# Performance work log

Measured on AMD Instinct MI355X. Metric: run time of the kernel, lower is better.

## Reference

```python
import jax, jax.numpy as jnp
import numpy as np

EPS = 1e-5
SCALE = 30.0

def _ln(x, g, b):
    mu = jnp.mean(x, -1, keepdims=True)
    var = jnp.mean((x - mu) ** 2, -1, keepdims=True)
    return (x - mu) / jnp.sqrt(var + EPS) * g + b

def _gather_nodes(h_V, E_idx):
    # h_V: [B,N,H], E_idx: [B,N,K] -> [B,N,K,H]
    return jax.vmap(lambda v, i: v[i])(h_V, E_idx)

def setup_inputs() -> dict:
    B, N, K, H, IN = 4, 2048, 48, 128, 128
    key = jax.random.key(0)
    ks = jax.random.split(key, 24)
    def lin(k, din, dout):
        kw, kb = jax.random.split(k)
        return (jax.random.normal(kw, (din, dout), jnp.float32) * 0.02,
                jax.random.normal(kb, (dout,), jnp.float32) * 0.02)
    W1_w, W1_b = lin(ks[0], H + IN, H)
    W2_w, W2_b = lin(ks[1], H, H)
    W3_w, W3_b = lin(ks[2], H, H)
    W11_w, W11_b = lin(ks[3], 2 * H + IN, H)
    W12_w, W12_b = lin(ks[4], H, H)
    W13_w, W13_b = lin(ks[5], H, IN)
    Win_w, Win_b = lin(ks[6], H, 4 * H)
    Wout_w, Wout_b = lin(ks[7], 4 * H, H)
    return {
        'h_V': jax.random.normal(ks[8], (B, N, H), jnp.float32),
        'h_E': jax.random.normal(ks[9], (B, N, K, IN), jnp.float32),
        'mask_V': jnp.ones((B, N), jnp.float32),
        'E_idx': jax.random.randint(ks[10], (B, N, K), 0, N),
        'mask_attend': jax.random.uniform(ks[11], (B, N, K), jnp.float32),
        'W1_w': W1_w, 'W1_b': W1_b, 'W2_w': W2_w, 'W2_b': W2_b,
        'W3_w': W3_w, 'W3_b': W3_b,
        'W11_w': W11_w, 'W11_b': W11_b, 'W12_w': W12_w, 'W12_b': W12_b,
        'W13_w': W13_w, 'W13_b': W13_b,
        'Win_w': Win_w, 'Win_b': Win_b, 'Wout_w': Wout_w, 'Wout_b': Wout_b,
        'ln1_g': jnp.ones((H,), jnp.float32), 'ln1_b': jnp.zeros((H,), jnp.float32),
        'ln2_g': jnp.ones((H,), jnp.float32), 'ln2_b': jnp.zeros((H,), jnp.float32),
        'ln3_g': jnp.ones((IN,), jnp.float32), 'ln3_b': jnp.zeros((IN,), jnp.float32),
    }

def reference(h_V, h_E, mask_V, E_idx, mask_attend,
              W1_w, W1_b, W2_w, W2_b, W3_w, W3_b,
              W11_w, W11_b, W12_w, W12_b, W13_w, W13_b,
              Win_w, Win_b, Wout_w, Wout_b,
              ln1_g, ln1_b, ln2_g, ln2_b, ln3_g, ln3_b):
    K = h_E.shape[-2]
    gelu = jax.nn.gelu
    # node message MLP over concat([h_V expanded, h_E])
    h_V_exp = jnp.broadcast_to(h_V[:, :, None, :], h_E.shape[:3] + (h_V.shape[-1],))
    h_EV = jnp.concatenate([h_V_exp, h_E], -1)  # [B,N,K,H+IN]
    h_msg = gelu(h_EV @ W1_w + W1_b)
    h_msg = gelu(h_msg @ W2_w + W2_b)
    h_msg = h_msg @ W3_w + W3_b
    h_msg = mask_attend[..., None] * h_msg
    dh = jnp.sum(h_msg, -2) / SCALE
    h_V = _ln(h_V + dh, ln1_g, ln1_b)  # dropout is identity in eval
    # FFN
    dh = gelu(h_V @ Win_w + Win_b) @ Wout_w + Wout_b
    h_V = _ln(h_V + dh, ln2_g, ln2_b)
    h_V = mask_V[..., None] * h_V
    # edge update: cat_neighbors_nodes = cat([h_E, gather(h_V, E_idx)], -1)
    h_nbr = _gather_nodes(h_V, E_idx)  # [B,N,K,H]
    h_EV2 = jnp.concatenate([h_E, h_nbr], -1)  # [B,N,K,IN+H]
    h_V_exp2 = jnp.broadcast_to(h_V[:, :, None, :], (h_V.shape[0], h_V.shape[1], K, h_V.shape[-1]))
    h_EV2 = jnp.concatenate([h_V_exp2, h_EV2], -1)  # [B,N,K,2H+IN]
    h_msg2 = gelu(h_EV2 @ W11_w + W11_b)
    h_msg2 = gelu(h_msg2 @ W12_w + W12_b)
    h_msg2 = h_msg2 @ W13_w + W13_b
    h_E = _ln(h_E + h_msg2, ln3_g, ln3_b)
    return (h_V, h_E)
```

## Files before the change

kernel.cpp:

```cpp
#include <hip/hip_runtime.h>
#include <stdint.h>


typedef __attribute__((ext_vector_type(8))) short bf16x8;
typedef __attribute__((ext_vector_type(4))) float f32x4;
typedef __attribute__((ext_vector_type(4))) float vf4;
typedef __attribute__((ext_vector_type(2))) float vf2;

#define MFMA16(a,b,c) __builtin_amdgcn_mfma_f32_16x16x32_bf16((a),(b),(c),0,0,0)
#define PITCH 17

__device__ __forceinline__ float bf2f(uint16_t u){
  union { uint32_t i; float f; } v; v.i = ((uint32_t)u) << 16; return v.f;
}
__device__ __forceinline__ uint32_t cvtpk(float lo, float hi){
  uint32_t r; asm("v_cvt_pk_bf16_f32 %0, %1, %2" : "=v"(r) : "v"(lo), "v"(hi));
  return r;
}
__device__ __forceinline__ uint16_t f2bf1(float x){ return (uint16_t)cvtpk(x, x); }
__device__ __forceinline__ uint4 pk8v(vf4 a, vf4 b){
  uint4 v; v.x=cvtpk(a[0],a[1]); v.y=cvtpk(a[2],a[3]);
  v.z=cvtpk(b[0],b[1]); v.w=cvtpk(b[2],b[3]); return v;
}
__device__ __forceinline__ float geluf(float x){
  float u = 0.7978845608028654f * x * fmaf(0.044715f, x*x, 1.0f);
  float e = __builtin_amdgcn_exp2f(2.8853900817779268f * u);
  float r = __builtin_amdgcn_rcpf(1.0f + e);
  return fmaf(-x, r, x);
}
template<int CTRL>
__device__ __forceinline__ float dpp_add(float x){
  int s = __builtin_amdgcn_update_dpp(0, __builtin_bit_cast(int, x), CTRL, 0xF, 0xF, true);
  return x + __builtin_bit_cast(float, s);
}
__device__ __forceinline__ float red16(float x){
  x = dpp_add<0x121>(x); x = dpp_add<0x122>(x);
  x = dpp_add<0x124>(x); x = dpp_add<0x128>(x);
  return x;
}
__device__ __forceinline__ bf16x8 wfragf(const float* __restrict__ W, int ncols,
                                         int k0, int col, int g){
  const float* p = W + (size_t)(k0 + g*8)*ncols + col;
  bf16x8 f;
#pragma unroll
  for (int j=0;j<8;j++) f[j] = (short)f2bf1(p[j*ncols]);
  return f;
}
__device__ __forceinline__ bf16x8 afrag(const uint4* tile, int row, int s, int g){
  return *(const bf16x8*)&tile[row*PITCH + 4*s + g];
}
__device__ __forceinline__ void st_m(uint4* tile, int row, int col, uint16_t val){
  ((uint16_t*)tile)[row*(PITCH*8) + col] = val;
}

__global__ __launch_bounds__(512) void k_node(
  const float* __restrict__ hV, const float* __restrict__ hE,
  const float* __restrict__ mAtt,
  const float* __restrict__ W1, const float* __restrict__ B1,
  const float* __restrict__ W2, const float* __restrict__ B2,
  const float* __restrict__ W3, const float* __restrict__ B3,
  const float* __restrict__ LG1, const float* __restrict__ LB1,
  float* __restrict__ x1f, uint16_t* __restrict__ x1b)
{
  __shared__ uint4 Ab[2][48*PITCH];
  __shared__ uint4 Cb[48*PITCH];
  __shared__ uint4 hvb[16];
  __shared__ float maskb[48];
  __shared__ float dhb[128];

  const int tid = threadIdx.x;
  const int w = tid >> 6, lane = tid & 63, g = lane >> 4, l15 = lane & 15;
  const int col = w*16 + l15;
  const int row0 = tid>>4, cir = tid&15, row1 = 32 + (tid>>4);

  bf16x8 W1f[8], W2f[4], W3f[4];
#pragma unroll
  for (int s=0;s<8;s++) W1f[s] = wfragf(W1,128,32*s,col,g);
#pragma unroll
  for (int s=0;s<4;s++) W2f[s] = wfragf(W2,128,32*s,col,g);
#pragma unroll
  for (int s=0;s<4;s++) W3f[s] = wfragf(W3,128,32*s,col,g);
  const float b1c = B1[col], b2c = B2[col], b3c = B3[col];

  vf4 sr0, sr1, sr2, sr3, hva, hvc; float mk = 0.f;
  {
    const float* hb = hE + (size_t)(blockIdx.x*8)*6144;
    sr0 = __builtin_nontemporal_load((const vf4*)(hb + tid*8));
    sr1 = __builtin_nontemporal_load((const vf4*)(hb + tid*8 + 4));
    if (tid < 256){
      sr2 = __builtin_nontemporal_load((const vf4*)(hb + 4096 + tid*8));
      sr3 = __builtin_nontemporal_load((const vf4*)(hb + 4096 + tid*8 + 4));
    }
    if (tid < 16){
      const float* p = hV + (size_t)(blockIdx.x*8)*128 + tid*8;
      hva = *(const vf4*)p; hvc = *(const vf4*)(p+4);
    }
    if (tid >= 64 && tid < 112) mk = mAtt[(size_t)(blockIdx.x*8)*48 + (tid-64)];
    Ab[0][row0*PITCH + cir] = pk8v(sr0, sr1);
    if (tid < 256) Ab[0][row1*PITCH + cir] = pk8v(sr2, sr3);
    if (tid < 16) hvb[tid] = pk8v(hva, hvc);
    if (tid >= 64 && tid < 112) maskb[tid-64] = mk;
  }
  __syncthreads();

  for (int it=0; it<8; ++it){
    const int node = blockIdx.x*8 + it;
    const uint4* Ac = Ab[it&1];
    uint4* Acm = Ab[it&1];
    uint4* An  = Ab[(it&1)^1];
    f32x4 ahv = {0,0,0,0};
#pragma unroll
    for (int s=0;s<4;s++) ahv = MFMA16(*(const bf16x8*)&hvb[4*s+g], W1f[s], ahv);
#pragma unroll
    for (int t=0;t<3;t++){
      f32x4 acc = ahv;
      int row = 16*t + l15;
#pragma unroll
      for (int s=0;s<4;s++) acc = MFMA16(afrag(Ac,row,s,g), W1f[4+s], acc);
#pragma unroll
      for (int r=0;r<4;r++) st_m(Cb, 16*t+4*g+r, col, f2bf1(geluf(acc[r]+b1c)));
    }
    __syncthreads();
#pragma unroll
    for (int t=0;t<3;t++){
      f32x4 acc = {0,0,0,0};
      int row = 16*t + l15;
#pragma unroll
      for (int s=0;s<4;s++) acc = MFMA16(afrag(Cb,row,s,g), W2f[s], acc);
#pragma unroll
      for (int r=0;r<4;r++) st_m(Acm, 16*t+4*g+r, col, f2bf1(geluf(acc[r]+b2c)));
    }
    __syncthreads();
    if (it < 7){
      const float* hb = hE + (size_t)(node+1)*6144;
      sr0 = __builtin_nontemporal_load((const vf4*)(hb + tid*8));
      sr1 = __builtin_nontemporal_load((const vf4*)(hb + tid*8 + 4));
      if (tid < 256){
        sr2 = __builtin_nontemporal_load((const vf4*)(hb + 4096 + tid*8));
        sr3 = __builtin_nontemporal_load((const vf4*)(hb + 4096 + tid*8 + 4));
      }
      if (tid < 16){
        const float* p = hV + (size_t)(node+1)*128 + tid*8;
        hva = *(const vf4*)p; hvc = *(const vf4*)(p+4);
      }
      if (tid >= 64 && tid < 112) mk = mAtt[(size_t)(node+1)*48 + (tid-64)];
    }
    float pp = 0.f;
#pragma unroll
    for (int t=0;t<3;t++){
      f32x4 acc = {0,0,0,0};
      int row = 16*t + l15;
#pragma unroll
      for (int s=0;s<4;s++) acc = MFMA16(afrag(Ac,row,s,g), W3f[s], acc);
#pragma unroll
      for (int r=0;r<4;r++) pp += maskb[16*t+4*g+r] * (acc[r] + b3c);
    }
    pp += __shfl_xor(pp, 16);
    pp += __shfl_xor(pp, 32);
    if (lane < 16) dhb[col] = pp * (1.f/30.f);
    __syncthreads();
    if (tid < 64){
      int c0 = 2*tid, c1 = c0+1;
      float2 hv2 = *(const float2*)(hV + (size_t)node*128 + c0);
      float xa = hv2.x + dhb[c0];
      float xc = hv2.y + dhb[c1];
      float s1 = xa + xc, s2 = xa*xa + xc*xc;
      s1 = red16(s1); s2 = red16(s2);
      s1 += __shfl_xor(s1,16); s2 += __shfl_xor(s2,16);
      s1 += __shfl_xor(s1,32); s2 += __shfl_xor(s2,32);
      float mu = s1 * (1.0f/128.0f);
      float var = fmaxf(s2 * (1.0f/128.0f) - mu*mu, 0.f);
      float rstd = __builtin_amdgcn_rsqf(var + 1e-5f);
      float ya = (xa-mu)*rstd*LG1[c0] + LB1[c0];
      float yc = (xc-mu)*rstd*LG1[c1] + LB1[c1];
      float2 o2; o2.x = ya; o2.y = yc;
      ((float2*)x1f)[(size_t)node*64 + tid] = o2;
      ((uint32_t*)x1b)[(size_t)node*64 + tid] = cvtpk(ya, yc);
    }
    if (it < 7){
      An[row0*PITCH + cir] = pk8v(sr0, sr1);
      if (tid < 256) An[row1*PITCH + cir] = pk8v(sr2, sr3);
      if (tid < 16) hvb[tid] = pk8v(hva, hvc);
      if (tid >= 64 && tid < 112) maskb[tid-64] = mk;
    }
    __syncthreads();
  }
}

__global__ __launch_bounds__(512) void k_ffn(
  const float* __restrict__ x1f, const uint16_t* __restrict__ x1b,
  const float* __restrict__ Win, const float* __restrict__ Bin,
  const float* __restrict__ Wout, const float* __restrict__ Bout,
  const float* __restrict__ LG2, const float* __restrict__ LB2,
  const float* __restrict__ maskV,
  float* __restrict__ outV, uint16_t* __restrict__ outVb)
{
  __shared__ uint4 lh[16*65];
  __shared__ float xb[16*129];

  const int tid = threadIdx.x;
  const int w = tid>>6, lane = tid&63, g = lane>>4, l15 = lane&15;
  const int colo = w*16 + l15;

  bf16x8 WiF[4][4], WoF[16];
#pragma unroll
  for (int s=0;s<4;s++)
#pragma unroll
    for (int c=0;c<4;c++) WiF[s][c] = wfragf(Win,512,32*s, w*64 + c*16 + l15, g);
#pragma unroll
  for (int s=0;s<16;s++) WoF[s] = wfragf(Wout,128,32*s, colo, g);
  float binc[4];
#pragma unroll
  for (int c=0;c<4;c++) binc[c] = Bin[w*64 + c*16 + l15];
  const float boutc = Bout[colo];

  for (int it=0; it<2; ++it){
    const int node0 = (blockIdx.x*2 + it)*16;
    bf16x8 A[4];
#pragma unroll
    for (int s=0;s<4;s++) A[s] = *(const bf16x8*)(x1b + (size_t)(node0 + l15)*128 + 32*s + 8*g);
#pragma unroll
    for (int c=0;c<4;c++){
      f32x4 acc = {0,0,0,0};
#pragma unroll
      for (int s=0;s<4;s++) acc = MFMA16(A[s], WiF[s][c], acc);
      int colh = w*64 + c*16 + l15;
#pragma unroll
      for (int r=0;r<4;r++){
        int row = 4*g + r;
        ((uint16_t*)lh)[row*(65*8) + colh] = f2bf1(geluf(acc[r] + binc[c]));
      }
    }
    __syncthreads();
    f32x4 acc = {0,0,0,0};
#pragma unroll
    for (int s=0;s<16;s++){
      bf16x8 a = *(const bf16x8*)&lh[l15*65 + 4*s + g];
      acc = MFMA16(a, WoF[s], acc);
    }
#pragma unroll
    for (int r=0;r<4;r++){
      int row = 4*g + r;
      xb[row*129 + colo] = x1f[(size_t)(node0+row)*128 + colo] + acc[r] + boutc;
    }
    __syncthreads();
#pragma unroll
    for (int rr=0; rr<2; ++rr){
      int row = w + rr*8;
      int c0 = 2*lane, c1 = c0+1;
      float xa = xb[row*129 + c0], xc = xb[row*129 + c1];
      float s1 = xa + xc, s2 = xa*xa + xc*xc;
      s1 = red16(s1); s2 = red16(s2);
      s1 += __shfl_xor(s1,16); s2 += __shfl_xor(s2,16);
      s1 += __shfl_xor(s1,32); s2 += __shfl_xor(s2,32);
      float mu = s1*(1.0f/128.0f);
      float var = fmaxf(s2*(1.0f/128.0f)-mu*mu, 0.f);
      float rstd = __builtin_amdgcn_rsqf(var + 1e-5f);
      float mv = maskV[node0 + row];
      float ya = ((xa-mu)*rstd*LG2[c0] + LB2[c0]) * mv;
      float yc = ((xc-mu)*rstd*LG2[c1] + LB2[c1]) * mv;
      vf2 o2; o2[0] = ya; o2[1] = yc;
      __builtin_nontemporal_store(o2, (vf2*)outV + (size_t)(node0+row)*64 + lane);
      if (outVb)
        ((uint32_t*)outVb)[(size_t)(node0+row)*64 + lane] = cvtpk(ya, yc);
    }
    __syncthreads();
  }
}

template<bool BF16G>
__global__ __launch_bounds__(512) void k_edge(
  const float* __restrict__ hE, const int* __restrict__ Eidx,
  const float* __restrict__ hV2f, const uint16_t* __restrict__ hV2b,
  const float* __restrict__ W11, const float* __restrict__ B11,
  const float* __restrict__ W12, const float* __restrict__ B12,
  const float* __restrict__ W13, const float* __restrict__ B13,
  const float* __restrict__ LG3, const float* __restrict__ LB3,
  float* __restrict__ outE)
{
  __shared__ uint4 Ab[2][48*PITCH];
  __shared__ uint4 Bb[48*PITCH];
  __shared__ uint4 Cb[48*PITCH];
  __shared__ uint4 hvb[16];

  const int tid = threadIdx.x;
  const int w = tid>>6, lane = tid&63, g = lane>>4, l15 = lane&15;
  const int col = w*16 + l15;
  const int row0 = tid>>4, cir = tid&15, row1 = 32 + (tid>>4);

  bf16x8 Ws[4], W11e[4], W11n[4], W12f[4], W13f[4];
#pragma unroll
  for (int s=0;s<4;s++) Ws[s]   = wfragf(W11,128,     32*s,col,g);
#pragma unroll
  for (int s=0;s<4;s++) W11e[s] = wfragf(W11,128, 128+32*s,col,g);
#pragma unroll
  for (int s=0;s<4;s++) W11n[s] = wfragf(W11,128, 256+32*s,col,g);
#pragma unroll
  for (int s=0;s<4;s++) W12f[s] = wfragf(W12,128,     32*s,col,g);
#pragma unroll
  for (int s=0;s<4;s++) W13f[s] = wfragf(W13,128,     32*s,col,g);
  const float b11c = B11[col], b12c = B12[col], b13c = B13[col];

  vf4 sr0, sr1, sr2, sr3; int gi0, gi1; uint4 hvr;
  {
    const int node = blockIdx.x*8;
    const int bb = (node >> 11) << 11;
    const float* hb = hE + (size_t)node*6144;
    sr0 = __builtin_nontemporal_load((const vf4*)(hb + tid*8));
    sr1 = __builtin_nontemporal_load((const vf4*)(hb + tid*8 + 4));
    if (tid < 256){
      sr2 = __builtin_nontemporal_load((const vf4*)(hb + 4096 + tid*8));
      sr3 = __builtin_nontemporal_load((const vf4*)(hb + 4096 + tid*8 + 4));
    }
    gi0 = Eidx[(size_t)node*48 + (tid>>4)];
    gi1 = (tid < 256) ? Eidx[(size_t)node*48 + 32 + (tid>>4)] : 0;
    uint4 gq0, gq1;
    if (BF16G){
      gq0 = *(const uint4*)(hV2b + (size_t)(bb + gi0)*128 + (tid&15)*8);
      if (tid < 256) gq1 = *(const uint4*)(hV2b + (size_t)(bb + gi1)*128 + (tid&15)*8);
      if (tid < 16) hvr = *(const uint4*)(hV2b + (size_t)node*128 + tid*8);
    } else {
      const float* p0 = hV2f + (size_t)(bb + gi0)*128 + (tid&15)*8;
      gq0 = pk8v(*(const vf4*)p0, *(const vf4*)(p0+4));
      if (tid < 256){
        const float* p1 = hV2f + (size_t)(bb + gi1)*128 + (tid&15)*8;
        gq1 = pk8v(*(const vf4*)p1, *(const vf4*)(p1+4));
      }
      if (tid < 16){
        const float* p = hV2f + (size_t)node*128 + tid*8;
        hvr = pk8v(*(const vf4*)p, *(const vf4*)(p+4));
      }
    }
    Ab[0][row0*PITCH + cir] = pk8v(sr0, sr1);
    Bb[row0*PITCH + cir] = gq0;
    if (tid < 256){
      Ab[0][row1*PITCH + cir] = pk8v(sr2, sr3);
      Bb[row1*PITCH + cir] = gq1;
    }
    if (tid < 16) hvb[tid] = hvr;
  }
  __syncthreads();

  for (int it=0; it<8; ++it){
    const int node = blockIdx.x*8 + it;
    const uint4* Ac = Ab[it&1];
    uint4* An = Ab[(it&1)^1];
    f32x4 ahv = {0,0,0,0};
#pragma unroll
    for (int s=0;s<4;s++) ahv = MFMA16(*(const bf16x8*)&hvb[4*s+g], Ws[s], ahv);
#pragma unroll
    for (int t=0;t<3;t++){
      f32x4 acc = ahv;
      int row = 16*t + l15;
#pragma unroll
      for (int s=0;s<4;s++) acc = MFMA16(afrag(Ac,row,s,g), W11e[s], acc);
#pragma unroll
      for (int s=0;s<4;s++) acc = MFMA16(afrag(Bb,row,s,g), W11n[s], acc);
#pragma unroll
      for (int r=0;r<4;r++) st_m(Cb, 16*t+4*g+r, col, f2bf1(geluf(acc[r]+b11c)));
    }
    __syncthreads();
#pragma unroll
    for (int t=0;t<3;t++){
      f32x4 acc = {0,0,0,0};
      int row = 16*t + l15;
#pragma unroll
      for (int s=0;s<4;s++) acc = MFMA16(afrag(Cb,row,s,g), W12f[s], acc);
#pragma unroll
      for (int r=0;r<4;r++) st_m(Bb, 16*t+4*g+r, col, f2bf1(geluf(acc[r]+b12c)));
    }
    __syncthreads();
    if (it < 7){
      const float* hb = hE + (size_t)(node+1)*6144;
      sr0 = __builtin_nontemporal_load((const vf4*)(hb + tid*8));
      sr1 = __builtin_nontemporal_load((const vf4*)(hb + tid*8 + 4));
      if (tid < 256){
        sr2 = __builtin_nontemporal_load((const vf4*)(hb + 4096 + tid*8));
        sr3 = __builtin_nontemporal_load((const vf4*)(hb + 4096 + tid*8 + 4));
      }
      gi0 = Eidx[(size_t)(node+1)*48 + (tid>>4)];
      gi1 = (tid < 256) ? Eidx[(size_t)(node+1)*48 + 32 + (tid>>4)] : 0;
    }
#pragma unroll
    for (int t=0;t<3;t++){
      f32x4 acc = {0,0,0,0};
      int row = 16*t + l15;
#pragma unroll
      for (int s=0;s<4;s++) acc = MFMA16(afrag(Bb,row,s,g), W13f[s], acc);
#pragma unroll
      for (int r=0;r<4;r++) st_m(Cb, 16*t+4*g+r, col, f2bf1(acc[r]+b13c));
    }
    __syncthreads();
    uint4 gq0, gq1;
    if (it < 7){
      const int bb2 = ((node+1) >> 11) << 11;
      if (BF16G){
        gq0 = *(const uint4*)(hV2b + (size_t)(bb2 + gi0)*128 + (tid&15)*8);
        if (tid < 256) gq1 = *(const uint4*)(hV2b + (size_t)(bb2 + gi1)*128 + (tid&15)*8);
        if (tid < 16) hvr = *(const uint4*)(hV2b + (size_t)(node+1)*128 + tid*8);
      } else {
        const float* p0 = hV2f + (size_t)(bb2 + gi0)*128 + (tid&15)*8;
        gq0 = pk8v(*(const vf4*)p0, *(const vf4*)(p0+4));
        if (tid < 256){
          const float* p1 = hV2f + (size_t)(bb2 + gi1)*128 + (tid&15)*8;
          gq1 = pk8v(*(const vf4*)p1, *(const vf4*)(p1+4));
        }
        if (tid < 16){
          const float* p = hV2f + (size_t)(node+1)*128 + tid*8;
          hvr = pk8v(*(const vf4*)p, *(const vf4*)(p+4));
        }
      }
    }
#pragma unroll
    for (int rr=0; rr<6; ++rr){
      int row = w + rr*8;
      int c0 = 2*lane;
      uint32_t pe = ((const uint32_t*)Ac)[row*(PITCH*4) + lane];
      uint32_t pv = ((const uint32_t*)Cb)[row*(PITCH*4) + lane];
      float xa = bf2f((uint16_t)(pe & 0xffff)) + bf2f((uint16_t)(pv & 0xffff));
      float xc = bf2f((uint16_t)(pe >> 16))    + bf2f((uint16_t)(pv >> 16));
      float s1 = xa + xc, s2 = xa*xa + xc*xc;
      s1 = red16(s1); s2 = red16(s2);
      s1 += __shfl_xor(s1,16); s2 += __shfl_xor(s2,16);
      s1 += __shfl_xor(s1,32); s2 += __shfl_xor(s2,32);
      float mu = s1*(1.0f/128.0f);
      float var = fmaxf(s2*(1.0f/128.0f)-mu*mu, 0.f);
      float rstd = __builtin_amdgcn_rsqf(var+1e-5f);
      float ya = (xa-mu)*rstd*LG3[c0] + LB3[c0];
      float yc = (xc-mu)*rstd*LG3[c0+1] + LB3[c0+1];
      vf2 o2; o2[0] = ya; o2[1] = yc;
      __builtin_nontemporal_store(o2, (vf2*)outE + ((size_t)node*48 + row)*64 + lane);
    }
    if (it < 7){
      An[row0*PITCH + cir] = pk8v(sr0, sr1);
      Bb[row0*PITCH + cir] = gq0;
      if (tid < 256){
        An[row1*PITCH + cir] = pk8v(sr2, sr3);
        Bb[row1*PITCH + cir] = gq1;
      }
      if (tid < 16) hvb[tid] = hvr;
    }
    __syncthreads();
  }
}

extern "C" void kernel_launch(void* const* d_in, const int* in_sizes, int n_in,
                              void* d_out, int out_size, void* d_ws, size_t ws_size,
                              hipStream_t stream){
  const float* hV   = (const float*)d_in[0];
  const float* hE   = (const float*)d_in[1];
  const float* mV   = (const float*)d_in[2];
  const int*   Eidx = (const int*)d_in[3];
  const float* mAtt = (const float*)d_in[4];
  const float* W1 = (const float*)d_in[5];  const float* B1 = (const float*)d_in[6];
  const float* W2 = (const float*)d_in[7];  const float* B2 = (const float*)d_in[8];
  const float* W3 = (const float*)d_in[9];  const float* B3 = (const float*)d_in[10];
  const float* W11 = (const float*)d_in[11]; const float* B11 = (const float*)d_in[12];
  const float* W12 = (const float*)d_in[13]; const float* B12 = (const float*)d_in[14];
  const float* W13 = (const float*)d_in[15]; const float* B13 = (const float*)d_in[16];
  const float* Win = (const float*)d_in[17]; const float* Bin = (const float*)d_in[18];
  const float* Wout= (const float*)d_in[19]; const float* Bout= (const float*)d_in[20];
  const float* LG1 = (const float*)d_in[21]; const float* LB1 = (const float*)d_in[22];
  const float* LG2 = (const float*)d_in[23]; const float* LB2 = (const float*)d_in[24];
  const float* LG3 = (const float*)d_in[25]; const float* LB3 = (const float*)d_in[26];

  float* outV = (float*)d_out;
  float* outE = outV + (size_t)1048576;
  float*    x1f = outE;
  uint16_t* x1b = (uint16_t*)(outE + (size_t)1048576);

  const bool bf16g = ws_size >= ((size_t)2<<20);
  uint16_t* outVb = bf16g ? (uint16_t*)d_ws : nullptr;

  hipLaunchKernelGGL(k_node, dim3(1024), dim3(512), 0, stream,
      hV, hE, mAtt, W1,B1, W2,B2, W3,B3, LG1,LB1, x1f, x1b);
  hipLaunchKernelGGL(k_ffn, dim3(256), dim3(512), 0, stream,
      x1f, x1b, Win,Bin, Wout,Bout, LG2,LB2, mV, outV, outVb);
  if (bf16g)
    hipLaunchKernelGGL((k_edge<true>), dim3(1024), dim3(512), 0, stream,
        hE, Eidx, outV, outVb, W11,B11, W12,B12, W13,B13, LG3,LB3, outE);
  else
    hipLaunchKernelGGL((k_edge<false>), dim3(1024), dim3(512), 0, stream,
        hE, Eidx, outV, nullptr, W11,B11, W12,B12, W13,B13, LG3,LB3, outE);
}
```

Measured before the change: 316.3 us.

## Precompute per-node hV@W1 and hV@W11 projections once instead of per edge

```diff
diff --git a/kernel.cpp b/kernel.cpp
--- a/kernel.cpp
+++ b/kernel.cpp
@@ -53,9 +53,34 @@
   ((uint16_t*)tile)[row*(PITCH*8) + col] = val;
 }
 
-__global__ __launch_bounds__(512) void k_node(
+__global__ __launch_bounds__(512) void k_pre(
+  const float* __restrict__ hV, const float* __restrict__ W1,
+  float* __restrict__ hvW1)
+{
+  const int tid = threadIdx.x;
+  const int w = tid>>6, lane = tid&63, g = lane>>4, l15 = lane&15;
+  const int col = w*16 + l15;
+  const int node0 = blockIdx.x*16;
+  bf16x8 Wf[4], A[4];
+#pragma unroll
+  for (int s=0;s<4;s++) Wf[s] = wfragf(W1,128,32*s,col,g);
+#pragma unroll
+  for (int s=0;s<4;s++){
+    const float* p = hV + (size_t)(node0 + l15)*128 + 32*s + 8*g;
+    uint4 t = pk8v(*(const vf4*)p, *(const vf4*)(p+4));
+    A[s] = __builtin_bit_cast(bf16x8, t);
+  }
+  f32x4 acc = {0,0,0,0};
+#pragma unroll
+  for (int s=0;s<4;s++) acc = MFMA16(A[s], Wf[s], acc);
+#pragma unroll
+  for (int r=0;r<4;r++) hvW1[(size_t)(node0 + 4*g + r)*128 + col] = acc[r];
+}
+
+__global__ __launch_bounds__(512) __attribute__((amdgpu_waves_per_eu(4,4)))
+void k_node(
   const float* __restrict__ hV, const float* __restrict__ hE,
-  const float* __restrict__ mAtt,
+  const float* __restrict__ mAtt, const float* __restrict__ hvW1,
   const float* __restrict__ W1, const float* __restrict__ B1,
   const float* __restrict__ W2, const float* __restrict__ B2,
   const float* __restrict__ W3, const float* __restrict__ B3,
@@ -64,7 +89,6 @@
 {
   __shared__ uint4 Ab[2][48*PITCH];
   __shared__ uint4 Cb[48*PITCH];
-  __shared__ uint4 hvb[16];
   __shared__ float maskb[48];
   __shared__ float dhb[128];
 
@@ -73,32 +97,31 @@
   const int col = w*16 + l15;
   const int row0 = tid>>4, cir = tid&15, row1 = 32 + (tid>>4);
 
-  bf16x8 W1f[8], W2f[4], W3f[4];
-#pragma unroll
-  for (int s=0;s<8;s++) W1f[s] = wfragf(W1,128,32*s,col,g);
+  bf16x8 W1e[4], W2f[4], W3f[4];
+#pragma unroll
+  for (int s=0;s<4;s++) W1e[s] = wfragf(W1,128,128+32*s,col,g);
 #pragma unroll
   for (int s=0;s<4;s++) W2f[s] = wfragf(W2,128,32*s,col,g);
 #pragma unroll
   for (int s=0;s<4;s++) W3f[s] = wfragf(W3,128,32*s,col,g);
   const float b1c = B1[col], b2c = B2[col], b3c = B3[col];
-
-  vf4 sr0, sr1, sr2, sr3, hva, hvc; float mk = 0.f;
+  float lg0 = 0, lg1 = 0, lb0 = 0, lb1 = 0;
+  if (tid < 64){ lg0 = LG1[2*tid]; lg1 = LG1[2*tid+1]; lb0 = LB1[2*tid]; lb1 = LB1[2*tid+1]; }
+
+  vf4 sr0, sr1, sr2, sr3; float mk = 0.f, hv1;
   {
-    const float* hb = hE + (size_t)(blockIdx.x*8)*6144;
+    const int node = blockIdx.x*8;
+    const float* hb = hE + (size_t)node*6144;
     sr0 = __builtin_nontemporal_load((const vf4*)(hb + tid*8));
     sr1 = __builtin_nontemporal_load((const vf4*)(hb + tid*8 + 4));
     if (tid < 256){
       sr2 = __builtin_nontemporal_load((const vf4*)(hb + 4096 + tid*8));
       sr3 = __builtin_nontemporal_load((const vf4*)(hb + 4096 + tid*8 + 4));
     }
-    if (tid < 16){
-      const float* p = hV + (size_t)(blockIdx.x*8)*128 + tid*8;
-      hva = *(const vf4*)p; hvc = *(const vf4*)(p+4);
-    }
-    if (tid >= 64 && tid < 112) mk = mAtt[(size_t)(blockIdx.x*8)*48 + (tid-64)];
+    if (tid >= 64 && tid < 112) mk = mAtt[(size_t)node*48 + (tid-64)];
+    hv1 = hvW1[(size_t)node*128 + col];
     Ab[0][row0*PITCH + cir] = pk8v(sr0, sr1);
     if (tid < 256) Ab[0][row1*PITCH + cir] = pk8v(sr2, sr3);
-    if (tid < 16) hvb[tid] = pk8v(hva, hvc);
     if (tid >= 64 && tid < 112) maskb[tid-64] = mk;
   }
   __syncthreads();
@@ -108,15 +131,13 @@
     const uint4* Ac = Ab[it&1];
     uint4* Acm = Ab[it&1];
     uint4* An  = Ab[(it&1)^1];
-    f32x4 ahv = {0,0,0,0};
-#pragma unroll
-    for (int s=0;s<4;s++) ahv = MFMA16(*(const bf16x8*)&hvb[4*s+g], W1f[s], ahv);
+    f32x4 ahv = {hv1, hv1, hv1, hv1};
 #pragma unroll
     for (int t=0;t<3;t++){
       f32x4 acc = ahv;
       int row = 16*t + l15;
 #pragma unroll
-      for (int s=0;s<4;s++) acc = MFMA16(afrag(Ac,row,s,g), W1f[4+s], acc);
+      for (int s=0;s<4;s++) acc = MFMA16(afrag(Ac,row,s,g), W1e[s], acc);
 #pragma unroll
       for (int r=0;r<4;r++) st_m(Cb, 16*t+4*g+r, col, f2bf1(geluf(acc[r]+b1c)));
     }
@@ -139,11 +160,8 @@
         sr2 = __builtin_nontemporal_load((const vf4*)(hb + 4096 + tid*8));
         sr3 = __builtin_nontemporal_load((const vf4*)(hb + 4096 + tid*8 + 4));
       }
-      if (tid < 16){
-        const float* p = hV + (size_t)(node+1)*128 + tid*8;
-        hva = *(const vf4*)p; hvc = *(const vf4*)(p+4);
-      }
       if (tid >= 64 && tid < 112) mk = mAtt[(size_t)(node+1)*48 + (tid-64)];
+      hv1 = hvW1[(size_t)(node+1)*128 + col];
     }
     float pp = 0.f;
 #pragma unroll
@@ -171,8 +189,8 @@
       float mu = s1 * (1.0f/128.0f);
       float var = fmaxf(s2 * (1.0f/128.0f) - mu*mu, 0.f);
       float rstd = __builtin_amdgcn_rsqf(var + 1e-5f);
-      float ya = (xa-mu)*rstd*LG1[c0] + LB1[c0];
-      float yc = (xc-mu)*rstd*LG1[c1] + LB1[c1];
+      float ya = (xa-mu)*rstd*lg0 + lb0;
+      float yc = (xc-mu)*rstd*lg1 + lb1;
       float2 o2; o2.x = ya; o2.y = yc;
       ((float2*)x1f)[(size_t)node*64 + tid] = o2;
       ((uint32_t*)x1b)[(size_t)node*64 + tid] = cvtpk(ya, yc);
@@ -180,20 +198,22 @@
     if (it < 7){
       An[row0*PITCH + cir] = pk8v(sr0, sr1);
       if (tid < 256) An[row1*PITCH + cir] = pk8v(sr2, sr3);
-      if (tid < 16) hvb[tid] = pk8v(hva, hvc);
       if (tid >= 64 && tid < 112) maskb[tid-64] = mk;
     }
     __syncthreads();
   }
 }
 
+template<bool HV11>
 __global__ __launch_bounds__(512) void k_ffn(
   const float* __restrict__ x1f, const uint16_t* __restrict__ x1b,
   const float* __restrict__ Win, const float* __restrict__ Bin,
   const float* __restrict__ Wout, const float* __restrict__ Bout,
+  const float* __restrict__ W11,
   const float* __restrict__ LG2, const float* __restrict__ LB2,
   const float* __restrict__ maskV,
-  float* __restrict__ outV, uint16_t* __restrict__ outVb)
+  float* __restrict__ outV, uint16_t* __restrict__ outVb,
+  float* __restrict__ hvW11)
 {
   __shared__ uint4 lh[16*65];
   __shared__ float xb[16*129];
@@ -202,17 +222,23 @@
   const int w = tid>>6, lane = tid&63, g = lane>>4, l15 = lane&15;
   const int colo = w*16 + l15;
 
-  bf16x8 WiF[4][4], WoF[16];
+  bf16x8 WiF[4][4], WoF[16], W11s[4];
 #pragma unroll
   for (int s=0;s<4;s++)
 #pragma unroll
     for (int c=0;c<4;c++) WiF[s][c] = wfragf(Win,512,32*s, w*64 + c*16 + l15, g);
 #pragma unroll
   for (int s=0;s<16;s++) WoF[s] = wfragf(Wout,128,32*s, colo, g);
+  if (HV11){
+#pragma unroll
+    for (int s=0;s<4;s++) W11s[s] = wfragf(W11,128,32*s,colo,g);
+  }
   float binc[4];
 #pragma unroll
   for (int c=0;c<4;c++) binc[c] = Bin[w*64 + c*16 + l15];
   const float boutc = Bout[colo];
+  const float lg0 = LG2[2*lane], lg1 = LG2[2*lane+1];
+  const float lb0 = LB2[2*lane], lb1 = LB2[2*lane+1];
 
   for (int it=0; it<2; ++it){
     const int node0 = (blockIdx.x*2 + it)*16;
@@ -247,8 +273,8 @@
 #pragma unroll
     for (int rr=0; rr<2; ++rr){
       int row = w + rr*8;
-      int c0 = 2*lane, c1 = c0+1;
-      float xa = xb[row*129 + c0], xc = xb[row*129 + c1];
+      int c0 = 2*lane;
+      float xa = xb[row*129 + c0], xc = xb[row*129 + c0 + 1];
       float s1 = xa + xc, s2 = xa*xa + xc*xc;
       s1 = red16(s1); s2 = red16(s2);
       s1 += __shfl_xor(s1,16); s2 += __shfl_xor(s2,16);
@@ -257,19 +283,179 @@
       float var = fmaxf(s2*(1.0f/128.0f)-mu*mu, 0.f);
       float rstd = __builtin_amdgcn_rsqf(var + 1e-5f);
       float mv = maskV[node0 + row];
-      float ya = ((xa-mu)*rstd*LG2[c0] + LB2[c0]) * mv;
-      float yc = ((xc-mu)*rstd*LG2[c1] + LB2[c1]) * mv;
+      float ya = ((xa-mu)*rstd*lg0 + lb0) * mv;
+      float yc = ((xc-mu)*rstd*lg1 + lb1) * mv;
       vf2 o2; o2[0] = ya; o2[1] = yc;
       __builtin_nontemporal_store(o2, (vf2*)outV + (size_t)(node0+row)*64 + lane);
+      uint32_t pk = cvtpk(ya, yc);
       if (outVb)
-        ((uint32_t*)outVb)[(size_t)(node0+row)*64 + lane] = cvtpk(ya, yc);
+        ((uint32_t*)outVb)[(size_t)(node0+row)*64 + lane] = pk;
+      if (HV11)
+        ((uint32_t*)lh)[row*132 + lane] = pk;
+    }
+    __syncthreads();
+    if (HV11){
+      f32x4 a2 = {0,0,0,0};
+#pragma unroll
+      for (int s=0;s<4;s++){
+        bf16x8 a = *(const bf16x8*)&((uint32_t*)lh)[l15*132 + 16*s + 4*g];
+        a2 = MFMA16(a, W11s[s], a2);
+      }
+#pragma unroll
+      for (int r=0;r<4;r++)
+        hvW11[(size_t)(node0 + 4*g + r)*128 + colo] = a2[r];
+      __syncthreads();
+    }
+  }
+}
+
+__global__ __launch_bounds__(512) __attribute__((amdgpu_waves_per_eu(4,4)))
+void k_edge_fast(
+  const float* __restrict__ hE, const int* __restrict__ Eidx,
+  const uint16_t* __restrict__ hV2b, const float* __restrict__ hvW11,
+  const float* __restrict__ W11, const float* __restrict__ B11,
+  const float* __restrict__ W12, const float* __restrict__ B12,
+  const float* __restrict__ W13, const float* __restrict__ B13,
+  const float* __restrict__ LG3, const float* __restrict__ LB3,
+  float* __restrict__ outE)
+{
+  __shared__ uint4 Ab[2][48*PITCH];
+  __shared__ uint4 Bb[48*PITCH];
+  __shared__ uint4 Cb[48*PITCH];
+
+  const int tid = threadIdx.x;
+  const int w = tid>>6, lane = tid&63, g = lane>>4, l15 = lane&15;
+  const int col = w*16 + l15;
+  const int row0 = tid>>4, cir = tid&15, row1 = 32 + (tid>>4);
+
+  bf16x8 W11e[4], W11n[4], W12f[4], W13f[4];
+#pragma unroll
+  for (int s=0;s<4;s++) W11e[s] = wfragf(W11,128, 128+32*s,col,g);
+#pragma unroll
+  for (int s=0;s<4;s++) W11n[s] = wfragf(W11,128, 256+32*s,col,g);
+#pragma unroll
+  for (int s=0;s<4;s++) W12f[s] = wfragf(W12,128,     32*s,col,g);
+#pragma unroll
+  for (int s=0;s<4;s++) W13f[s] = wfragf(W13,128,     32*s,col,g);
+  const float b11c = B11[col], b12c = B12[col], b13c = B13[col];
+  const float lg0 = LG3[2*lane], lg1 = LG3[2*lane+1];
+  const float lb0 = LB3[2*lane], lb1 = LB3[2*lane+1];
+
+  vf4 sr0, sr1, sr2, sr3; int gi0, gi1; float hv11;
+  {
+    const int node = blockIdx.x*8;
+    const int bb = (node >> 11) << 11;
+    const float* hb = hE + (size_t)node*6144;
+    sr0 = __builtin_nontemporal_load((const vf4*)(hb + tid*8));
+    sr1 = __builtin_nontemporal_load((const vf4*)(hb + tid*8 + 4));
+    if (tid < 256){
+      sr2 = __builtin_nontemporal_load((const vf4*)(hb + 4096 + tid*8));
+      sr3 = __builtin_nontemporal_load((const vf4*)(hb + 4096 + tid*8 + 4));
+    }
+    gi0 = Eidx[(size_t)node*48 + (tid>>4)];
+    gi1 = (tid < 256) ? Eidx[(size_t)node*48 + 32 + (tid>>4)] : 0;
+    hv11 = hvW11[(size_t)node*128 + col];
+    uint4 gq0 = *(const uint4*)(hV2b + (size_t)(bb + gi0)*128 + (tid&15)*8);
+    uint4 gq1;
+    if (tid < 256) gq1 = *(const uint4*)(hV2b + (size_t)(bb + gi1)*128 + (tid&15)*8);
+    Ab[0][row0*PITCH + cir] = pk8v(sr0, sr1);
+    Bb[row0*PITCH + cir] = gq0;
+    if (tid < 256){
+      Ab[0][row1*PITCH + cir] = pk8v(sr2, sr3);
+      Bb[row1*PITCH + cir] = gq1;
+    }
+  }
+  __syncthreads();
+
+  for (int it=0; it<8; ++it){
+    const int node = blockIdx.x*8 + it;
+    const uint4* Ac = Ab[it&1];
+    uint4* An = Ab[(it&1)^1];
+    f32x4 ahv = {hv11, hv11, hv11, hv11};
+#pragma unroll
+    for (int t=0;t<3;t++){
+      f32x4 acc = ahv;
+      int row = 16*t + l15;
+#pragma unroll
+      for (int s=0;s<4;s++) acc = MFMA16(afrag(Ac,row,s,g), W11e[s], acc);
+#pragma unroll
+      for (int s=0;s<4;s++) acc = MFMA16(afrag(Bb,row,s,g), W11n[s], acc);
+#pragma unroll
+      for (int r=0;r<4;r++) st_m(Cb, 16*t+4*g+r, col, f2bf1(geluf(acc[r]+b11c)));
+    }
+    __syncthreads();
+#pragma unroll
+    for (int t=0;t<3;t++){
+      f32x4 acc = {0,0,0,0};
+      int row = 16*t + l15;
+#pragma unroll
+      for (int s=0;s<4;s++) acc = MFMA16(afrag(Cb,row,s,g), W12f[s], acc);
+#pragma unroll
+      for (int r=0;r<4;r++) st_m(Bb, 16*t+4*g+r, col, f2bf1(geluf(acc[r]+b12c)));
+    }
+    __syncthreads();
+    if (it < 7){
+      const float* hb = hE + (size_t)(node+1)*6144;
+      sr0 = __builtin_nontemporal_load((const vf4*)(hb + tid*8));
+      sr1 = __builtin_nontemporal_load((const vf4*)(hb + tid*8 + 4));
+      if (tid < 256){
+        sr2 = __builtin_nontemporal_load((const vf4*)(hb + 4096 + tid*8));
+        sr3 = __builtin_nontemporal_load((const vf4*)(hb + 4096 + tid*8 + 4));
+      }
+      gi0 = Eidx[(size_t)(node+1)*48 + (tid>>4)];
+      gi1 = (tid < 256) ? Eidx[(size_t)(node+1)*48 + 32 + (tid>>4)] : 0;
+      hv11 = hvW11[(size_t)(node+1)*128 + col];
+    }
+#pragma unroll
+    for (int t=0;t<3;t++){
+      f32x4 acc = {0,0,0,0};
+      int row = 16*t + l15;
+#pragma unroll
+      for (int s=0;s<4;s++) acc = MFMA16(afrag(Bb,row,s,g), W13f[s], acc);
+#pragma unroll
+      for (int r=0;r<4;r++) st_m(Cb, 16*t+4*g+r, col, f2bf1(acc[r]+b13c));
+    }
+    __syncthreads();
+    uint4 gq0, gq1;
+    if (it < 7){
+      const int bb2 = ((node+1) >> 11) << 11;
+      gq0 = *(const uint4*)(hV2b + (size_t)(bb2 + gi0)*128 + (tid&15)*8);
+      if (tid < 256) gq1 = *(const uint4*)(hV2b + (size_t)(bb2 + gi1)*128 + (tid&15)*8);
+    }
+#pragma unroll
+    for (int rr=0; rr<6; ++rr){
+      int row = w + rr*8;
+      int c0 = 2*lane;
+      uint32_t pe = ((const uint32_t*)Ac)[row*(PITCH*4) + lane];
+      uint32_t pv = ((const uint32_t*)Cb)[row*(PITCH*4) + lane];
+      float xa = bf2f((uint16_t)(pe & 0xffff)) + bf2f((uint16_t)(pv & 0xffff));
+      float xc = bf2f((uint16_t)(pe >> 16))    + bf2f((uint16_t)(pv >> 16));
+      float s1 = xa + xc, s2 = xa*xa + xc*xc;
+      s1 = red16(s1); s2 = red16(s2);
+      s1 += __shfl_xor(s1,16); s2 += __shfl_xor(s2,16);
+      s1 += __shfl_xor(s1,32); s2 += __shfl_xor(s2,32);
+      float mu = s1*(1.0f/128.0f);
+      float var = fmaxf(s2*(1.0f/128.0f)-mu*mu, 0.f);
+      float rstd = __builtin_amdgcn_rsqf(var+1e-5f);
+      float ya = (xa-mu)*rstd*lg0 + lb0;
+      float yc = (xc-mu)*rstd*lg1 + lb1;
+      vf2 o2; o2[0] = ya; o2[1] = yc;
+      __builtin_nontemporal_store(o2, (vf2*)outE + ((size_t)node*48 + row)*64 + lane);
+    }
+    if (it < 7){
+      An[row0*PITCH + cir] = pk8v(sr0, sr1);
+      Bb[row0*PITCH + cir] = gq0;
+      if (tid < 256){
+        An[row1*PITCH + cir] = pk8v(sr2, sr3);
+        Bb[row1*PITCH + cir] = gq1;
+      }
     }
     __syncthreads();
   }
 }
 
 template<bool BF16G>
-__global__ __launch_bounds__(512) void k_edge(
+__global__ __launch_bounds__(512) void k_edge_safe(
   const float* __restrict__ hE, const int* __restrict__ Eidx,
   const float* __restrict__ hV2f, const uint16_t* __restrict__ hV2b,
   const float* __restrict__ W11, const float* __restrict__ B11,
@@ -468,18 +654,29 @@
   float* outE = outV + (size_t)1048576;
   float*    x1f = outE;
   uint16_t* x1b = (uint16_t*)(outE + (size_t)1048576);
+  float*    hvW1 = outE + (size_t)1572864;
 
   const bool bf16g = ws_size >= ((size_t)2<<20);
+  const bool fast  = ws_size >= ((size_t)6<<20);
   uint16_t* outVb = bf16g ? (uint16_t*)d_ws : nullptr;
-
+  float*    hvW11 = fast ? (float*)((char*)d_ws + ((size_t)2<<20)) : nullptr;
+
+  hipLaunchKernelGGL(k_pre, dim3(512), dim3(512), 0, stream, hV, W1, hvW1);
   hipLaunchKernelGGL(k_node, dim3(1024), dim3(512), 0, stream,
-      hV, hE, mAtt, W1,B1, W2,B2, W3,B3, LG1,LB1, x1f, x1b);
-  hipLaunchKernelGGL(k_ffn, dim3(256), dim3(512), 0, stream,
-      x1f, x1b, Win,Bin, Wout,Bout, LG2,LB2, mV, outV, outVb);
-  if (bf16g)
-    hipLaunchKernelGGL((k_edge<true>), dim3(1024), dim3(512), 0, stream,
-        hE, Eidx, outV, outVb, W11,B11, W12,B12, W13,B13, LG3,LB3, outE);
-  else
-    hipLaunchKernelGGL((k_edge<false>), dim3(1024), dim3(512), 0, stream,
-        hE, Eidx, outV, nullptr, W11,B11, W12,B12, W13,B13, LG3,LB3, outE);
-}
+      hV, hE, mAtt, hvW1, W1,B1, W2,B2, W3,B3, LG1,LB1, x1f, x1b);
+  if (fast){
+    hipLaunchKernelGGL((k_ffn<true>), dim3(256), dim3(512), 0, stream,
+        x1f, x1b, Win,Bin, Wout,Bout, W11, LG2,LB2, mV, outV, outVb, hvW11);
+    hipLaunchKernelGGL(k_edge_fast, dim3(1024), dim3(512), 0, stream,
+        hE, Eidx, outVb, hvW11, W11,B11, W12,B12, W13,B13, LG3,LB3, outE);
+  } else {
+    hipLaunchKernelGGL((k_ffn<false>), dim3(256), dim3(512), 0, stream,
+        x1f, x1b, Win,Bin, Wout,Bout, W11, LG2,LB2, mV, outV, outVb, nullptr);
+    if (bf16g)
+      hipLaunchKernelGGL((k_edge_safe<true>), dim3(1024), dim3(512), 0, stream,
+          hE, Eidx, outV, outVb, W11,B11, W12,B12, W13,B13, LG3,LB3, outE);
+    else
+      hipLaunchKernelGGL((k_edge_safe<false>), dim3(1024), dim3(512), 0, stream,
+          hE, Eidx, outV, nullptr, W11,B11, W12,B12, W13,B13, LG3,LB3, outE);
+  }
+}
```

Result: slower. 374.3 us (+18.3%).
